# Performance work log

Hardware: AMD Instinct MI355X
Metric: run time of the kernel (lower is better)

Reference implementation:

```python
import jax, jax.numpy as jnp
import numpy as np
from jax import lax


def setup_inputs() -> dict:
    key = jax.random.key(0)
    k1, k2, k3 = jax.random.split(key, 3)
    X = jax.random.normal(k1, (8192, 8192), dtype=jnp.float32)
    K = jax.random.normal(k2, (7, 7), dtype=jnp.float32)
    bias = jax.random.normal(k3, (1,), dtype=jnp.float32)
    return {"X": X, "K": K, "bias": bias}


def reference(X, K, bias):
    # Valid 2D cross-correlation of X [H, W] with K [kh, kw], plus scalar bias.
    # Output shape: [H - kh + 1, W - kw + 1].
    lhs = X[None, None, :, :]          # NCHW, N=C=1
    rhs = K[None, None, :, :]          # OIHW, O=I=1
    out = lax.conv_general_dilated(
        lhs, rhs,
        window_strides=(1, 1),
        padding='VALID',
        dimension_numbers=('NCHW', 'OIHW', 'NCHW'),
    )
    return out[0, 0] + bias[0]
```

## Files before the change

kernel.cpp:

```cpp
#include <hip/hip_runtime.h>
#include <hip/hip_bf16.h>

#define IN_N   8192
#define OUT_N  8186
#define KS     7

#define BXO    128
#define BYO    64
#define IC     144
#define IR     70
#define LSTR   304
#define GPR    36
#define NGRAN  (IR * GPR)
#define NLD    10
#define NSTEP  4
#define NSTRIP 64
#define NSEG   32

typedef __bf16 bf16x8 __attribute__((ext_vector_type(8)));
typedef float  f32x4  __attribute__((ext_vector_type(4)));

union BFU { __bf16 h; unsigned short u; };
__device__ __forceinline__ unsigned short f2bf(float f) {
    BFU c; c.h = (__bf16)f; return c.u;
}

template<bool GUARD>
__device__ __forceinline__ void run_block(
    const float* __restrict__ X, const float* __restrict__ Kw,
    const float* __restrict__ bias, float* __restrict__ out,
    char* sb0, char* sb1, int X0, int ybase, int tid)
{
    const int lane = tid & 63;
    const int w    = tid >> 6;
    const int lo   = lane & 15;
    const int hi   = lane >> 4;

    bf16x8 bfrag[KS];
    #pragma unroll
    for (int ky = 0; ky < KS; ++ky) {
        bf16x8 bv;
        #pragma unroll
        for (int e = 0; e < 8; ++e) {
            const int d = 8*hi + e - lo;
            const float v = (d >= 0 && d < KS) ? Kw[ky*KS + d] : 0.0f;
            bv[e] = (__bf16)v;
        }
        bfrag[ky] = bv;
    }
    const float b = bias[0];

    int srow[NLD], scol[NLD];
    #pragma unroll
    for (int k = 0; k < NLD; ++k) {
        const int g = k*256 + tid;
        srow[k] = g / GPR;
        scol[k] = (g - srow[k]*GPR) * 4;
    }

    {
        float4 ld[NLD];
        #pragma unroll
        for (int k = 0; k < NLD; ++k) {
            if (k*256 + tid < NGRAN) {
                int r = ybase + srow[k], c = X0 + scol[k];
                if (GUARD) { r = min(r, IN_N-1); c = min(c, IN_N-4); }
                ld[k] = *(const float4*)(X + (size_t)r * IN_N + c);
            }
        }
        #pragma unroll
        for (int k = 0; k < NLD; ++k) {
            if (k*256 + tid < NGRAN) {
                ushort4 h;
                h.x = f2bf(ld[k].x); h.y = f2bf(ld[k].y);
                h.z = f2bf(ld[k].z); h.w = f2bf(ld[k].w);
                *(ushort4*)( (k & 1 ? sb0 : sb0) + srow[k]*LSTR + scol[k]*2 ) = h;
            }
        }
    }
    asm volatile("s_waitcnt lgkmcnt(0)" ::: "memory");
    __builtin_amdgcn_s_barrier();
    __builtin_amdgcn_sched_barrier(0);

    #pragma unroll
    for (int t = 0; t < NSTEP; ++t) {
        char* cur = (t & 1) ? sb1 : sb0;
        char* nxt = (t & 1) ? sb0 : sb1;
        const int y0 = ybase + t * BYO;

        float4 ld[NLD];
        if (t + 1 < NSTEP) {
            const int yn = y0 + BYO;
            #pragma unroll
            for (int k = 0; k < NLD; ++k) {
                if (k*256 + tid < NGRAN) {
                    int r = yn + srow[k], c = X0 + scol[k];
                    if (GUARD) { r = min(r, IN_N-1); c = min(c, IN_N-4); }
                    ld[k] = *(const float4*)(X + (size_t)r * IN_N + c);
                }
            }
        }

        const char* abase = cur + (16*w + lo) * LSTR + 16*hi;
        float* obase = out + (size_t)(y0 + 16*w + 4*hi) * OUT_N + (X0 + lo);
        #pragma unroll
        for (int t8 = 0; t8 < 8; ++t8) {
            f32x4 acc = { b, b, b, b };
            #pragma unroll
            for (int ky = 0; ky < KS; ++ky) {
                bf16x8 a = *(const bf16x8*)(abase + ky*LSTR + 32*t8);
                acc = __builtin_amdgcn_mfma_f32_16x16x32_bf16(a, bfrag[ky], acc, 0, 0, 0);
            }
            if (GUARD) {
                const int ox = X0 + 16*t8 + lo;
                if (ox < OUT_N) {
                    #pragma unroll
                    for (int r = 0; r < 4; ++r) {
                        const int oy = y0 + 16*w + 4*hi + r;
                        if (oy < OUT_N) obase[(size_t)r*OUT_N + 16*t8] = acc[r];
                    }
                }
            } else {
                #pragma unroll
                for (int r = 0; r < 4; ++r)
                    obase[(size_t)r*OUT_N + 16*t8] = acc[r];
            }
        }

        if (t + 1 < NSTEP) {
            #pragma unroll
            for (int k = 0; k < NLD; ++k) {
                if (k*256 + tid < NGRAN) {
                    ushort4 h;
                    h.x = f2bf(ld[k].x); h.y = f2bf(ld[k].y);
                    h.z = f2bf(ld[k].z); h.w = f2bf(ld[k].w);
                    *(ushort4*)(nxt + srow[k]*LSTR + scol[k]*2) = h;
                }
            }
            asm volatile("s_waitcnt lgkmcnt(0)" ::: "memory");
            __builtin_amdgcn_s_barrier();
            __builtin_amdgcn_sched_barrier(0);
        }
    }
}

__global__ __launch_bounds__(256, 3)
void conv7x7_mfma(const float* __restrict__ X, const float* __restrict__ Kw,
                  const float* __restrict__ bias, float* __restrict__ out) {
    __shared__ __align__(16) char sb[2][IR * LSTR];
    const int tid = threadIdx.x;

    const int bid = blockIdx.x;
    const int swz = (bid & 7) * (NSTRIP * NSEG / 8) + (bid >> 3);
    const int strip = swz & (NSTRIP - 1);
    const int seg   = swz >> 6;
    const int X0    = strip * BXO;
    const int ybase = seg * (BYO * NSTEP);

    if (strip == NSTRIP-1 || seg == NSEG-1)
        run_block<true >(X, Kw, bias, out, sb[0], sb[1], X0, ybase, tid);
    else
        run_block<false>(X, Kw, bias, out, sb[0], sb[1], X0, ybase, tid);
}

extern "C" void kernel_launch(void* const* d_in, const int* in_sizes, int n_in,
                              void* d_out, int out_size, void* d_ws, size_t ws_size,
                              hipStream_t stream) {
    const float* X    = (const float*)d_in[0];
    const float* Kw   = (const float*)d_in[1];
    const float* bias = (const float*)d_in[2];
    float* out = (float*)d_out;

    conv7x7_mfma<<<dim3(NSTRIP * NSEG), dim3(256), 0, stream>>>(X, Kw, bias, out);
}
```

Baseline: 146.7 us.

## Halve row tile height, split waves 2x2, and use dual MFMA accumulators

Shrinks each step's row tile from 64 to 32 rows and doubles the number of segments. Waves are rearranged in a 2x2 grid over the 32x128 output tile, and each wave now does 4 column tiles instead of 8. The 7-tap MFMA chain is split across two accumulators to shorten the dependency chain, with all A loads hoisted ahead. Smaller LDS buffers allow the launch-bounds occupancy target to rise from 3 to 6 blocks. The cost is more halo reloading: 38 input rows are staged per 32 output rows, where before it was 70 per 64.

```diff
diff --git a/kernel.cpp b/kernel.cpp
--- a/kernel.cpp
+++ b/kernel.cpp
@@ -6,16 +6,17 @@
 #define KS     7
 
 #define BXO    128
-#define BYO    64
+#define BYO    32
 #define IC     144
-#define IR     70
+#define IR     38
 #define LSTR   304
 #define GPR    36
 #define NGRAN  (IR * GPR)
-#define NLD    10
+#define NLD    6
 #define NSTEP  4
+#define SEG_ROWS (BYO * NSTEP)
+#define NSEG   64
 #define NSTRIP 64
-#define NSEG   32
 
 typedef __bf16 bf16x8 __attribute__((ext_vector_type(8)));
 typedef float  f32x4  __attribute__((ext_vector_type(4)));
@@ -32,7 +33,9 @@
     char* sb0, char* sb1, int X0, int ybase, int tid)
 {
     const int lane = tid & 63;
-    const int w    = tid >> 6;
+    const int wv   = tid >> 6;
+    const int wy   = wv & 1;
+    const int wx   = wv >> 1;
     const int lo   = lane & 15;
     const int hi   = lane >> 4;
 
@@ -43,8 +46,7 @@
         #pragma unroll
         for (int e = 0; e < 8; ++e) {
             const int d = 8*hi + e - lo;
-            const float v = (d >= 0 && d < KS) ? Kw[ky*KS + d] : 0.0f;
-            bv[e] = (__bf16)v;
+            bv[e] = (__bf16)((d >= 0 && d < KS) ? Kw[ky*KS + d] : 0.0f);
         }
         bfrag[ky] = bv;
     }
@@ -74,7 +76,7 @@
                 ushort4 h;
                 h.x = f2bf(ld[k].x); h.y = f2bf(ld[k].y);
                 h.z = f2bf(ld[k].z); h.w = f2bf(ld[k].w);
-                *(ushort4*)( (k & 1 ? sb0 : sb0) + srow[k]*LSTR + scol[k]*2 ) = h;
+                *(ushort4*)(sb0 + srow[k]*LSTR + scol[k]*2) = h;
             }
         }
     }
@@ -101,22 +103,34 @@
             }
         }
 
-        const char* abase = cur + (16*w + lo) * LSTR + 16*hi;
-        float* obase = out + (size_t)(y0 + 16*w + 4*hi) * OUT_N + (X0 + lo);
+        const char* abase = cur + (16*wy + lo) * LSTR + 128*wx + 16*hi;
+        float* obase = out + (size_t)(y0 + 16*wy + 4*hi) * OUT_N + (X0 + 64*wx + lo);
         #pragma unroll
-        for (int t8 = 0; t8 < 8; ++t8) {
-            f32x4 acc = { b, b, b, b };
-            #pragma unroll
-            for (int ky = 0; ky < KS; ++ky) {
-                bf16x8 a = *(const bf16x8*)(abase + ky*LSTR + 32*t8);
-                acc = __builtin_amdgcn_mfma_f32_16x16x32_bf16(a, bfrag[ky], acc, 0, 0, 0);
-            }
+        for (int t8 = 0; t8 < 4; ++t8) {
+            f32x4 accA = { b, b, b, b };
+            f32x4 accB = { 0.f, 0.f, 0.f, 0.f };
+            bf16x8 a0 = *(const bf16x8*)(abase + 0*LSTR + 32*t8);
+            bf16x8 a1 = *(const bf16x8*)(abase + 1*LSTR + 32*t8);
+            bf16x8 a2 = *(const bf16x8*)(abase + 2*LSTR + 32*t8);
+            bf16x8 a3 = *(const bf16x8*)(abase + 3*LSTR + 32*t8);
+            bf16x8 a4 = *(const bf16x8*)(abase + 4*LSTR + 32*t8);
+            bf16x8 a5 = *(const bf16x8*)(abase + 5*LSTR + 32*t8);
+            bf16x8 a6 = *(const bf16x8*)(abase + 6*LSTR + 32*t8);
+            accA = __builtin_amdgcn_mfma_f32_16x16x32_bf16(a0, bfrag[0], accA, 0, 0, 0);
+            accB = __builtin_amdgcn_mfma_f32_16x16x32_bf16(a1, bfrag[1], accB, 0, 0, 0);
+            accA = __builtin_amdgcn_mfma_f32_16x16x32_bf16(a2, bfrag[2], accA, 0, 0, 0);
+            accB = __builtin_amdgcn_mfma_f32_16x16x32_bf16(a3, bfrag[3], accB, 0, 0, 0);
+            accA = __builtin_amdgcn_mfma_f32_16x16x32_bf16(a4, bfrag[4], accA, 0, 0, 0);
+            accB = __builtin_amdgcn_mfma_f32_16x16x32_bf16(a5, bfrag[5], accB, 0, 0, 0);
+            accA = __builtin_amdgcn_mfma_f32_16x16x32_bf16(a6, bfrag[6], accA, 0, 0, 0);
+            const f32x4 acc = accA + accB;
+
             if (GUARD) {
-                const int ox = X0 + 16*t8 + lo;
+                const int ox = X0 + 64*wx + 16*t8 + lo;
                 if (ox < OUT_N) {
                     #pragma unroll
                     for (int r = 0; r < 4; ++r) {
-                        const int oy = y0 + 16*w + 4*hi + r;
+                        const int oy = y0 + 16*wy + 4*hi + r;
                         if (oy < OUT_N) obase[(size_t)r*OUT_N + 16*t8] = acc[r];
                     }
                 }
@@ -144,7 +158,7 @@
     }
 }
 
-__global__ __launch_bounds__(256, 3)
+__global__ __launch_bounds__(256, 6)
 void conv7x7_mfma(const float* __restrict__ X, const float* __restrict__ Kw,
                   const float* __restrict__ bias, float* __restrict__ out) {
     __shared__ __align__(16) char sb[2][IR * LSTR];
@@ -155,7 +169,7 @@
     const int strip = swz & (NSTRIP - 1);
     const int seg   = swz >> 6;
     const int X0    = strip * BXO;
-    const int ybase = seg * (BYO * NSTEP);
+    const int ybase = seg * SEG_ROWS;
 
     if (strip == NSTRIP-1 || seg == NSEG-1)
         run_block<true >(X, Kw, bias, out, sb[0], sb[1], X0, ybase, tid);
```

Result: slower. 286.9 us (+95.6%).

## Restructure conv into wide persistent strips with rolling LDS row buffer

Applied to the files above, without the earlier changes.

Replaces 128x256 output tiles with 765 blocks, each sweeping a 496-column-wide strip down a range of 16-row steps. Input rows live in a 40-row circular LDS buffer, so each step loads only 16 new rows. This cuts the halo re-reads caused by the narrow tiles. It also swaps the MFMA operand roles so each lane writes contiguous float2 pairs, splits the 7-tap chain across two accumulators, and rebalances the block-to-XCD mapping. The costs are lower per-block parallelism, one barrier per 16-row step, and the 31 column tiles not dividing evenly over 4 waves.

```diff
diff --git a/kernel.cpp b/kernel.cpp
--- a/kernel.cpp
+++ b/kernel.cpp
@@ -1,21 +1,19 @@
 #include <hip/hip_runtime.h>
 #include <hip/hip_bf16.h>
 
-#define IN_N   8192
-#define OUT_N  8186
-#define KS     7
+#define IN_N    8192
+#define OUT_N   8186
+#define KS      7
 
-#define BXO    128
-#define BYO    64
-#define IC     144
-#define IR     70
-#define LSTR   304
-#define GPR    36
-#define NGRAN  (IR * GPR)
-#define NLD    10
-#define NSTEP  4
-#define NSTRIP 64
-#define NSEG   32
+#define SCOLS   512
+#define OCOLS   496
+#define NSTRIP  17
+#define NSEG    45
+#define NBLK    (NSTRIP * NSEG)
+#define NROWB   40
+#define LSTR    1040
+#define NT8     31
+#define TOTSTEP 512
 
 typedef __bf16 bf16x8 __attribute__((ext_vector_type(8)));
 typedef float  f32x4  __attribute__((ext_vector_type(4)));
@@ -25,16 +23,139 @@
     BFU c; c.h = (__bf16)f; return c.u;
 }
 
-template<bool GUARD>
-__device__ __forceinline__ void run_block(
-    const float* __restrict__ X, const float* __restrict__ Kw,
-    const float* __restrict__ bias, float* __restrict__ out,
-    char* sb0, char* sb1, int X0, int ybase, int tid)
+template<bool G>
+__device__ __forceinline__ void run_strip(
+    const float* __restrict__ X, float* __restrict__ out,
+    char* sb, const bf16x8* bfrag, float bv,
+    int X0, int s0, int s1, int tid)
 {
     const int lane = tid & 63;
-    const int w    = tid >> 6;
+    const int wv   = tid >> 6;
     const int lo   = lane & 15;
     const int hi   = lane >> 4;
+    const int p    = tid >> 7;
+    const int cg   = tid & 127;
+    const int ccol = X0 + 4 * cg;
+    const int wcol = cg * 8;
+
+    int wbase = (16 * s0 + 22 + p) % NROWB;
+
+    int roff[KS];
+    #pragma unroll
+    for (int ky = 0; ky < KS; ++ky)
+        roff[ky] = ((16 * s0 + lo + ky) % NROWB) * LSTR + 16 * hi;
+
+    #pragma unroll
+    for (int k = 0; k < 11; ++k) {
+        int r = 16 * s0 + 2 * k + p;
+        int c = ccol;
+        if (G) { r = min(r, IN_N - 1); c = min(c, IN_N - 4); }
+        float4 v = *(const float4*)(X + (size_t)r * IN_N + c);
+        ushort4 h;
+        h.x = f2bf(v.x); h.y = f2bf(v.y); h.z = f2bf(v.z); h.w = f2bf(v.w);
+        const int slot = (16 * s0 + 2 * k + p) % NROWB;
+        *(ushort4*)(sb + slot * LSTR + wcol) = h;
+    }
+    asm volatile("s_waitcnt lgkmcnt(0)" ::: "memory");
+    __builtin_amdgcn_s_barrier();
+    __builtin_amdgcn_sched_barrier(0);
+
+    float4 ld[8];
+    for (int s = s0; s < s1; ++s) {
+        const int Y = 16 * s;
+        const bool pre = (s + 1 < s1);
+
+        if (pre) {
+            #pragma unroll
+            for (int k = 0; k < 8; ++k) {
+                int r = Y + 22 + 2 * k + p;
+                int c = ccol;
+                if (G) { r = min(r, IN_N - 1); c = min(c, IN_N - 4); }
+                ld[k] = *(const float4*)(X + (size_t)r * IN_N + c);
+            }
+        }
+        __builtin_amdgcn_sched_barrier(0);
+
+        for (int t8 = wv; t8 < NT8; t8 += 4) {
+            const int off = 32 * t8;
+            f32x4 accA = { bv, bv, bv, bv };
+            f32x4 accB = { 0.f, 0.f, 0.f, 0.f };
+            bf16x8 a0 = *(const bf16x8*)(sb + roff[0] + off);
+            bf16x8 a1 = *(const bf16x8*)(sb + roff[1] + off);
+            bf16x8 a2 = *(const bf16x8*)(sb + roff[2] + off);
+            bf16x8 a3 = *(const bf16x8*)(sb + roff[3] + off);
+            bf16x8 a4 = *(const bf16x8*)(sb + roff[4] + off);
+            bf16x8 a5 = *(const bf16x8*)(sb + roff[5] + off);
+            bf16x8 a6 = *(const bf16x8*)(sb + roff[6] + off);
+            accA = __builtin_amdgcn_mfma_f32_16x16x32_bf16(bfrag[0], a0, accA, 0, 0, 0);
+            accB = __builtin_amdgcn_mfma_f32_16x16x32_bf16(bfrag[1], a1, accB, 0, 0, 0);
+            accA = __builtin_amdgcn_mfma_f32_16x16x32_bf16(bfrag[2], a2, accA, 0, 0, 0);
+            accB = __builtin_amdgcn_mfma_f32_16x16x32_bf16(bfrag[3], a3, accB, 0, 0, 0);
+            accA = __builtin_amdgcn_mfma_f32_16x16x32_bf16(bfrag[4], a4, accA, 0, 0, 0);
+            accB = __builtin_amdgcn_mfma_f32_16x16x32_bf16(bfrag[5], a5, accB, 0, 0, 0);
+            accA = __builtin_amdgcn_mfma_f32_16x16x32_bf16(bfrag[6], a6, accA, 0, 0, 0);
+            const f32x4 acc = accA + accB;
+
+            const int oy = Y + lo;
+            const int ox = X0 + 16 * t8 + 4 * hi;
+            if constexpr (!G) {
+                float2* po = (float2*)(out + (size_t)oy * OUT_N + ox);
+                po[0] = make_float2(acc[0], acc[1]);
+                po[1] = make_float2(acc[2], acc[3]);
+            } else {
+                if (oy < OUT_N) {
+                    #pragma unroll
+                    for (int r = 0; r < 4; ++r)
+                        if (ox + r < OUT_N) out[(size_t)oy * OUT_N + ox + r] = acc[r];
+                }
+            }
+        }
+        __builtin_amdgcn_sched_barrier(0);
+
+        if (pre) {
+            #pragma unroll
+            for (int k = 0; k < 8; ++k) {
+                ushort4 h;
+                h.x = f2bf(ld[k].x); h.y = f2bf(ld[k].y);
+                h.z = f2bf(ld[k].z); h.w = f2bf(ld[k].w);
+                int slot = wbase + 2 * k;
+                if (slot >= NROWB) slot -= NROWB;
+                *(ushort4*)(sb + slot * LSTR + wcol) = h;
+            }
+            asm volatile("s_waitcnt lgkmcnt(0)" ::: "memory");
+            __builtin_amdgcn_s_barrier();
+            __builtin_amdgcn_sched_barrier(0);
+        }
+
+        wbase += 16; if (wbase >= NROWB) wbase -= NROWB;
+        #pragma unroll
+        for (int ky = 0; ky < KS; ++ky) {
+            roff[ky] += 16 * LSTR;
+            if (roff[ky] >= NROWB * LSTR) roff[ky] -= NROWB * LSTR;
+        }
+    }
+}
+
+__global__ __launch_bounds__(256, 3)
+void conv7x7_roll(const float* __restrict__ X, const float* __restrict__ Kw,
+                  const float* __restrict__ bias, float* __restrict__ out) {
+    __shared__ __align__(16) char sb[NROWB * LSTR];
+
+    const int tid  = threadIdx.x;
+    const int lane = tid & 63;
+    const int lo   = lane & 15;
+    const int hi   = lane >> 4;
+
+    const int orig = blockIdx.x;
+    const int xcd  = orig & 7;
+    const int idx  = orig >> 3;
+    const int wg   = (xcd < 5 ? xcd * 96 : 5 * 96 + (xcd - 5) * 95) + idx;
+    const int seg   = wg / NSTRIP;
+    const int strip = wg - seg * NSTRIP;
+
+    const int X0 = strip * OCOLS;
+    const int s0 = (TOTSTEP * seg) / NSEG;
+    const int s1 = (TOTSTEP * (seg + 1)) / NSEG;
 
     bf16x8 bfrag[KS];
     #pragma unroll
@@ -42,125 +163,17 @@
         bf16x8 bv;
         #pragma unroll
         for (int e = 0; e < 8; ++e) {
-            const int d = 8*hi + e - lo;
-            const float v = (d >= 0 && d < KS) ? Kw[ky*KS + d] : 0.0f;
-            bv[e] = (__bf16)v;
+            const int d = 8 * hi + e - lo;
+            bv[e] = (__bf16)((d >= 0 && d < KS) ? Kw[ky * KS + d] : 0.0f);
         }
         bfrag[ky] = bv;
     }
     const float b = bias[0];
 
-    int srow[NLD], scol[NLD];
-    #pragma unroll
-    for (int k = 0; k < NLD; ++k) {
-        const int g = k*256 + tid;
-        srow[k] = g / GPR;
-        scol[k] = (g - srow[k]*GPR) * 4;
-    }
-
-    {
-        float4 ld[NLD];
-        #pragma unroll
-        for (int k = 0; k < NLD; ++k) {
-            if (k*256 + tid < NGRAN) {
-                int r = ybase + srow[k], c = X0 + scol[k];
-                if (GUARD) { r = min(r, IN_N-1); c = min(c, IN_N-4); }
-                ld[k] = *(const float4*)(X + (size_t)r * IN_N + c);
-            }
-        }
-        #pragma unroll
-        for (int k = 0; k < NLD; ++k) {
-            if (k*256 + tid < NGRAN) {
-                ushort4 h;
-                h.x = f2bf(ld[k].x); h.y = f2bf(ld[k].y);
-                h.z = f2bf(ld[k].z); h.w = f2bf(ld[k].w);
-                *(ushort4*)( (k & 1 ? sb0 : sb0) + srow[k]*LSTR + scol[k]*2 ) = h;
-            }
-        }
-    }
-    asm volatile("s_waitcnt lgkmcnt(0)" ::: "memory");
-    __builtin_amdgcn_s_barrier();
-    __builtin_amdgcn_sched_barrier(0);
-
-    #pragma unroll
-    for (int t = 0; t < NSTEP; ++t) {
-        char* cur = (t & 1) ? sb1 : sb0;
-        char* nxt = (t & 1) ? sb0 : sb1;
-        const int y0 = ybase + t * BYO;
-
-        float4 ld[NLD];
-        if (t + 1 < NSTEP) {
-            const int yn = y0 + BYO;
-            #pragma unroll
-            for (int k = 0; k < NLD; ++k) {
-                if (k*256 + tid < NGRAN) {
-                    int r = yn + srow[k], c = X0 + scol[k];
-                    if (GUARD) { r = min(r, IN_N-1); c = min(c, IN_N-4); }
-                    ld[k] = *(const float4*)(X + (size_t)r * IN_N + c);
-                }
-            }
-        }
-
-        const char* abase = cur + (16*w + lo) * LSTR + 16*hi;
-        float* obase = out + (size_t)(y0 + 16*w + 4*hi) * OUT_N + (X0 + lo);
-        #pragma unroll
-        for (int t8 = 0; t8 < 8; ++t8) {
-            f32x4 acc = { b, b, b, b };
-            #pragma unroll
-            for (int ky = 0; ky < KS; ++ky) {
-                bf16x8 a = *(const bf16x8*)(abase + ky*LSTR + 32*t8);
-                acc = __builtin_amdgcn_mfma_f32_16x16x32_bf16(a, bfrag[ky], acc, 0, 0, 0);
-            }
-            if (GUARD) {
-                const int ox = X0 + 16*t8 + lo;
-                if (ox < OUT_N) {
-                    #pragma unroll
-                    for (int r = 0; r < 4; ++r) {
-                        const int oy = y0 + 16*w + 4*hi + r;
-                        if (oy < OUT_N) obase[(size_t)r*OUT_N + 16*t8] = acc[r];
-                    }
-                }
-            } else {
-                #pragma unroll
-                for (int r = 0; r < 4; ++r)
-                    obase[(size_t)r*OUT_N + 16*t8] = acc[r];
-            }
-        }
-
-        if (t + 1 < NSTEP) {
-            #pragma unroll
-            for (int k = 0; k < NLD; ++k) {
-                if (k*256 + tid < NGRAN) {
-                    ushort4 h;
-                    h.x = f2bf(ld[k].x); h.y = f2bf(ld[k].y);
-                    h.z = f2bf(ld[k].z); h.w = f2bf(ld[k].w);
-                    *(ushort4*)(nxt + srow[k]*LSTR + scol[k]*2) = h;
-                }
-            }
-            asm volatile("s_waitcnt lgkmcnt(0)" ::: "memory");
-            __builtin_amdgcn_s_barrier();
-            __builtin_amdgcn_sched_barrier(0);
-        }
-    }
-}
-
-__global__ __launch_bounds__(256, 3)
-void conv7x7_mfma(const float* __restrict__ X, const float* __restrict__ Kw,
-                  const float* __restrict__ bias, float* __restrict__ out) {
-    __shared__ __align__(16) char sb[2][IR * LSTR];
-    const int tid = threadIdx.x;
-
-    const int bid = blockIdx.x;
-    const int swz = (bid & 7) * (NSTRIP * NSEG / 8) + (bid >> 3);
-    const int strip = swz & (NSTRIP - 1);
-    const int seg   = swz >> 6;
-    const int X0    = strip * BXO;
-    const int ybase = seg * (BYO * NSTEP);
-
-    if (strip == NSTRIP-1 || seg == NSEG-1)
-        run_block<true >(X, Kw, bias, out, sb[0], sb[1], X0, ybase, tid);
+    if (strip < NSTRIP - 1 && seg < NSEG - 1)
+        run_strip<false>(X, out, sb, bfrag, b, X0, s0, s1, tid);
     else
-        run_block<false>(X, Kw, bias, out, sb[0], sb[1], X0, ybase, tid);
+        run_strip<true >(X, out, sb, bfrag, b, X0, s0, s1, tid);
 }
 
 extern "C" void kernel_launch(void* const* d_in, const int* in_sizes, int n_in,
@@ -171,5 +184,5 @@
     const float* bias = (const float*)d_in[2];
     float* out = (float*)d_out;
 
-    conv7x7_mfma<<<dim3(NSTRIP * NSEG), dim3(256), 0, stream>>>(X, Kw, bias, out);
+    conv7x7_roll<<<dim3(NBLK), dim3(256), 0, stream>>>(X, Kw, bias, out);
 }
```

After: 141.3 us (median of 2 runs). -3.7%, faster.
